# Optimization experiments

Measured on AMD Instinct MI355X. Metric: run time of the kernel, lower is better.

## Reference

```python
import jax, jax.numpy as jnp
import numpy as np

N = 4096          # num_nodes
F = 64            # node_features
H = 128           # hidden_dim
NH = 4            # num_heads
HD = H // NH      # per-head dim = 32
L = 3             # num_layers
C = 7             # num_classes
EDGE_P = 0.004    # ~16 avg degree


def setup_inputs() -> dict:
    key = jax.random.key(0)
    ks = jax.random.split(key, 20)
    g = lambda k, shape, fan_in: jax.random.normal(k, shape, jnp.float32) / np.sqrt(fan_in)
    x = jax.random.normal(ks[0], (N, F), jnp.float32)
    adj = (jax.random.uniform(ks[1], (N, N)) < EDGE_P).astype(jnp.float32)
    return {
        "x": x,
        "adj": adj,
        "enc_W": g(ks[2], (F, H), F), "enc_b": jnp.zeros((H,), jnp.float32),
        "gcn_W": g(ks[3], (L, H, H), H), "gcn_b": jnp.zeros((L, H), jnp.float32),
        "attn_W": g(ks[4], (L, NH, H, HD), H), "attn_Wb": jnp.zeros((L, NH, HD), jnp.float32),
        "attn_a": g(ks[5], (L, NH, 2 * HD), 2 * HD), "attn_ab": jnp.zeros((L, NH), jnp.float32),
        "cls_W1": g(ks[6], (H, H // 2), H), "cls_b1": jnp.zeros((H // 2,), jnp.float32),
        "cls_W2": g(ks[7], (H // 2, C), H // 2), "cls_b2": jnp.zeros((C,), jnp.float32),
        "con_W1": g(ks[8], (H, H // 2), H), "con_b1": jnp.zeros((H // 2,), jnp.float32),
        "con_W2": g(ks[9], (H // 2, 1), H // 2), "con_b2": jnp.zeros((1,), jnp.float32),
    }


def _normalize_adj(adj):
    a = adj + jnp.eye(adj.shape[0], dtype=adj.dtype)
    dinv = jnp.sum(a, axis=1) ** -0.5
    return dinv[:, None] * a * dinv[None, :]


def _gcn(h, adj_norm, W, b):
    support = adj_norm @ h                      # [N,H]
    return jax.nn.relu(support @ W + b)         # dropout=0 (eval)


def _attention(h, edge_mask, W, Wb, a, ab):
    # h:[N,H], W:[NH,H,HD], a:[NH,2*HD]; per-pair score = Linear(concat(h_i,h_j))
    hh = jnp.einsum('nf,hfd->hnd', h, W) + Wb[:, None, :]     # [NH,N,HD]
    a_src, a_dst = a[:, :HD], a[:, HD:]
    s_src = jnp.einsum('hnd,hd->hn', hh, a_src)               # [NH,N]
    s_dst = jnp.einsum('hnd,hd->hn', hh, a_dst)               # [NH,N]
    scores = s_src[:, :, None] + s_dst[:, None, :] + ab[:, None, None]
    # original uses literal 0.0 (NOT -inf) for non-edges before softmax
    scores = jnp.where(edge_mask[None, :, :], scores, 0.0)    # [NH,N,N]
    probs = jax.nn.softmax(scores, axis=-1)
    out = jnp.einsum('hij,hjd->hid', probs, hh)               # [NH,N,HD]
    return out.transpose(1, 0, 2).reshape(h.shape[0], NH * HD)


def reference(x, adj, enc_W, enc_b, gcn_W, gcn_b, attn_W, attn_Wb, attn_a, attn_ab,
              cls_W1, cls_b1, cls_W2, cls_b2, con_W1, con_b1, con_W2, con_b2):
    h = jax.nn.relu(x @ enc_W + enc_b)          # node encoder (dropout=0)
    adj_norm = _normalize_adj(adj)
    edge_mask = adj > 0
    for i in range(L):
        h_gcn = _gcn(h, adj_norm, gcn_W[i], gcn_b[i])
        h_attn = _attention(h, edge_mask, attn_W[i], attn_Wb[i], attn_a[i], attn_ab[i])
        h = jax.nn.relu(h_gcn + h_attn)
    node_logits = jax.nn.relu(h @ cls_W1 + cls_b1) @ cls_W2 + cls_b2
    h_mean = jnp.mean(h, axis=0, keepdims=True)
    contagion = jax.nn.relu(h_mean @ con_W1 + con_b1) @ con_W2 + con_b2
    return (node_logits, h, contagion)
```

## Files before the change

### kernel.cpp

```cpp
#include <hip/hip_runtime.h>

typedef unsigned short u16;
typedef unsigned int u32;

#define N 4096
#define F 64
#define H 128
#define NH 4
#define HD 32
#define EMAX 64

__device__ float g_hA[N * H];
__device__ float g_hB[N * H];
__device__ float g_hhA[N * H];
__device__ float g_hhB[N * H];
__device__ u16   g_cols[N * EMAX];
__device__ int   g_deg[N];
__device__ float g_dinv[N];
__device__ float g_ssrcA[N * NH];
__device__ float g_ssrcB[N * NH];
__device__ float g_sdstA[N * NH];
__device__ float g_sdstB[N * NH];
__device__ float g_part[4][32][H];
__device__ float g_gWQ[3 * H * H];
__device__ float g_aWQ[3 * NH * H * HD];
__device__ float g_W1Q[H * 64];

__device__ __forceinline__ void agg4(int i0, int tid, const float* __restrict__ h,
                                     const float* __restrict__ hhin,
                                     const float* __restrict__ ssrc_in,
                                     const float* __restrict__ sdst_in,
                                     int l, const float* __restrict__ abv,
                                     int (&jl)[4][EMAX], float (&dv)[4][EMAX],
                                     float (&sdl)[4][EMAX * NH], float (&wl)[4][EMAX * NH],
                                     float (&eml)[4][NH], float (&basel)[4][NH],
                                     float (&Svl)[4][NH],
                                     float& outa0, float& outa1,
                                     float& sup0, float& sup1) {
  int c = tid & 127, rg = tid >> 7, hc = c >> 5;
#pragma unroll
  for (int r = 0; r < 4; ++r) {
    int dd = g_deg[i0 + r];
    const u16* cl = g_cols + (size_t)(i0 + r) * EMAX;
    for (int e = tid; e < dd; e += 256) {
      int j = cl[e];
      jl[r][e] = j;
      dv[r][e] = g_dinv[j];
    }
  }
  __syncthreads();

  {
    int g = tid >> 4, lg = tid & 15, ra = g >> 2, ha = g & 3;
    int dda = g_deg[i0 + ra];
    float M = -INFINITY;
    for (int e = lg; e < dda; e += 16) {
      float s = sdst_in[jl[ra][e] * NH + ha];
      sdl[ra][e * NH + ha] = s;
      M = fmaxf(M, s);
    }
#pragma unroll
    for (int m = 8; m >= 1; m >>= 1) M = fmaxf(M, __shfl_xor(M, m, 64));
    if (lg == 0) {
      float ssrc = ssrc_in[(i0 + ra) * NH + ha];
      float ab = abv[ha];
      float mv = fmaxf(0.f, ssrc + ab + M);
      eml[ra][ha] = expf(-mv);
      basel[ra][ha] = ssrc + ab - mv;
    }
  }
  __syncthreads();

  {
    int g = tid >> 4, lg = tid & 15, ra = g >> 2, ha = g & 3;
    int dda = g_deg[i0 + ra];
    float base = basel[ra][ha];
    float Sp = 0.f;
    for (int e = lg; e < dda; e += 16) {
      float w = expf(base + sdl[ra][e * NH + ha]);
      wl[ra][e * NH + ha] = w;
      Sp += w;
    }
#pragma unroll
    for (int m = 8; m >= 1; m >>= 1) Sp += __shfl_xor(Sp, m, 64);
    if (lg == 0) Svl[ra][ha] = Sp;
  }
  __syncthreads();

  float sumc = 0.f;
  const float* part = &g_part[l][0][0];
#pragma unroll
  for (int s = 0; s < 32; ++s) sumc += part[s * H + c];

  float oa[2], sp[2];
#pragma unroll
  for (int rr = 0; rr < 2; ++rr) {
    int r = rg * 2 + rr;
    int i = i0 + r;
    int dd = g_deg[i];
    float em = eml[r][hc], S = Svl[r][hc];
    float aA = 0.f, aT = 0.f, aG = 0.f;
    int e = 0;
    for (; e + 4 <= dd; e += 4) {
      int j0 = jl[r][e], j1 = jl[r][e + 1], j2 = jl[r][e + 2], j3 = jl[r][e + 3];
      float w0 = wl[r][e * NH + hc],       w1 = wl[r][(e + 1) * NH + hc];
      float w2 = wl[r][(e + 2) * NH + hc], w3 = wl[r][(e + 3) * NH + hc];
      float q0 = hhin[j0 * H + c], q1 = hhin[j1 * H + c];
      float q2 = hhin[j2 * H + c], q3 = hhin[j3 * H + c];
      float p0 = h[j0 * H + c], p1 = h[j1 * H + c];
      float p2 = h[j2 * H + c], p3 = h[j3 * H + c];
      aA = fmaf(w0, q0, aA); aA = fmaf(w1, q1, aA);
      aA = fmaf(w2, q2, aA); aA = fmaf(w3, q3, aA);
      aT += (q0 + q1) + (q2 + q3);
      aG = fmaf(dv[r][e], p0, aG);     aG = fmaf(dv[r][e + 1], p1, aG);
      aG = fmaf(dv[r][e + 2], p2, aG); aG = fmaf(dv[r][e + 3], p3, aG);
    }
    for (; e < dd; ++e) {
      int j = jl[r][e];
      float w = wl[r][e * NH + hc];
      float q = hhin[j * H + c];
      aA = fmaf(w, q, aA);
      aT += q;
      aG = fmaf(dv[r][e], h[j * H + c], aG);
    }
    float Z = S + em * (float)(N - dd);
    oa[rr] = (aA + em * (sumc - aT)) / Z;
    float di = g_dinv[i];
    sp[rr] = di * (aG + di * h[i * H + c]);
  }
  outa0 = oa[0]; outa1 = oa[1]; sup0 = sp[0]; sup1 = sp[1];
}

__device__ __forceinline__ void proj4(int i0, int tid, const float (&hrowT)[H][4],
                                      const float* __restrict__ aW,
                                      const float* __restrict__ aWb,
                                      const float* __restrict__ aa, int lp,
                                      float* __restrict__ hhout,
                                      float* __restrict__ ssrc_out,
                                      float* __restrict__ sdst_out) {
  int c = tid & 127, rg = tid >> 7, hc = c >> 5, dc = c & 31;
  float b = aWb[hc * HD + dc];
  float p0 = b, p1 = b;
  for (int f = 0; f < H; ++f) {
    float w = aW[(hc * H + f) * HD + dc];
    float2 hv = *reinterpret_cast<const float2*>(&hrowT[f][rg * 2]);
    p0 = fmaf(hv.x, w, p0);
    p1 = fmaf(hv.y, w, p1);
  }
  int r0 = i0 + rg * 2, r1 = r0 + 1;
  hhout[r0 * H + c] = p0;
  hhout[r1 * H + c] = p1;
  const float* ap = aa + hc * 2 * HD;
  float as = ap[dc], ad = ap[HD + dc];
  float ss0 = p0 * as, ss1 = p1 * as, sd0 = p0 * ad, sd1 = p1 * ad;
#pragma unroll
  for (int m = 16; m >= 1; m >>= 1) {
    ss0 += __shfl_xor(ss0, m, 64); ss1 += __shfl_xor(ss1, m, 64);
    sd0 += __shfl_xor(sd0, m, 64); sd1 += __shfl_xor(sd1, m, 64);
  }
  if (dc == 0) {
    ssrc_out[r0 * NH + hc] = ss0; ssrc_out[r1 * NH + hc] = ss1;
    sdst_out[r0 * NH + hc] = sd0; sdst_out[r1 * NH + hc] = sd1;
  }
  atomicAdd(&g_part[lp][r0 & 31][c], p0);
  atomicAdd(&g_part[lp][r1 & 31][c], p1);
}

__global__ void k_csr_enc(const float* __restrict__ adj, const float* __restrict__ x,
                          const float* __restrict__ eW, const float* __restrict__ eb,
                          const float* __restrict__ aW, const float* __restrict__ aWb,
                          const float* __restrict__ aa, const float* __restrict__ gW,
                          const float* __restrict__ W1) {
  __shared__ float xT[F][4];
  __shared__ float hrowT[H][4];
  __shared__ int cnt;
  int tid = threadIdx.x;
  if (blockIdx.x < N) {
    int row = blockIdx.x;
    if (tid == 0) cnt = 0;
    __syncthreads();
    int base = tid * 16;
    const float4* p = reinterpret_cast<const float4*>(adj + (size_t)row * N + base);
    float4 q0 = p[0], q1 = p[1], q2 = p[2], q3 = p[3];
    float vals[16] = {q0.x, q0.y, q0.z, q0.w, q1.x, q1.y, q1.z, q1.w,
                      q2.x, q2.y, q2.z, q2.w, q3.x, q3.y, q3.z, q3.w};
#pragma unroll
    for (int t = 0; t < 16; ++t)
      if (vals[t] != 0.f) {
        int pos = atomicAdd(&cnt, 1);
        if (pos < EMAX) g_cols[row * EMAX + pos] = (u16)(base + t);
      }
    __syncthreads();
    if (tid == 0) {
      g_deg[row] = cnt < EMAX ? cnt : EMAX;
      g_dinv[row] = 1.0f / sqrtf((float)(cnt + 1));
    }
  } else if (blockIdx.x < N + N / 4) {
    int i0 = (blockIdx.x - N) * 4;
    int c = tid & 127, rg = tid >> 7;
    {
      int r = tid >> 6, k = tid & 63;
      xT[k][r] = x[(i0 + r) * F + k];
    }
    __syncthreads();
    float b = eb[c];
    float e0 = b, e1 = b;
    for (int k = 0; k < F; ++k) {
      float w = eW[k * H + c];
      float2 xv = *reinterpret_cast<const float2*>(&xT[k][rg * 2]);
      e0 = fmaf(xv.x, w, e0);
      e1 = fmaf(xv.y, w, e1);
    }
    e0 = fmaxf(e0, 0.f); e1 = fmaxf(e1, 0.f);
    int r0 = i0 + rg * 2, r1 = r0 + 1;
    g_hA[r0 * H + c] = e0; g_hA[r1 * H + c] = e1;
    hrowT[c][rg * 2] = e0; hrowT[c][rg * 2 + 1] = e1;
    __syncthreads();
    proj4(i0, tid, hrowT, aW, aWb, aa, 0, g_hhA, g_ssrcA, g_sdstA);
  } else {
    int gid = (blockIdx.x - (N + N / 4)) * 256 + tid;
    if (gid < 3 * H * H) {
      int l = gid / (H * H), rem = gid % (H * H);
      int fq = rem >> 9, c = (rem >> 2) & 127, ft = rem & 3;
      g_gWQ[gid] = gW[(size_t)l * H * H + (4 * fq + ft) * H + c];
      int hc = c >> 5, dc = c & 31;
      g_aWQ[gid] = aW[(((size_t)l * NH + hc) * H + (4 * fq + ft)) * HD + dc];
      if (gid < H * 64) {
        int fq2 = gid >> 8, u = (gid >> 2) & 63, ft2 = gid & 3;
        g_W1Q[gid] = W1[(4 * fq2 + ft2) * 64 + u];
      }
    }
  }
}

__device__ __forceinline__ void gemm2q(const float* __restrict__ s0,
                                       const float* __restrict__ s1,
                                       const float4* __restrict__ wq,
                                       float& a0, float& a1) {
#pragma unroll 4
  for (int fq = 0; fq < 32; ++fq) {
    float4 w  = wq[fq * 128];
    float4 v0 = *reinterpret_cast<const float4*>(s0 + fq * 4);
    float4 v1 = *reinterpret_cast<const float4*>(s1 + fq * 4);
    a0 = fmaf(v0.x, w.x, a0); a0 = fmaf(v0.y, w.y, a0);
    a0 = fmaf(v0.z, w.z, a0); a0 = fmaf(v0.w, w.w, a0);
    a1 = fmaf(v1.x, w.x, a1); a1 = fmaf(v1.y, w.y, a1);
    a1 = fmaf(v1.z, w.z, a1); a1 = fmaf(v1.w, w.w, a1);
  }
}

__device__ __forceinline__ void proj4q(int i0, int tid, const float (&hT)[4][H],
                                       const float4* __restrict__ aq,
                                       const float* __restrict__ aWb,
                                       const float* __restrict__ aa, int lp,
                                       float* __restrict__ hhout,
                                       float* __restrict__ ssrc_out,
                                       float* __restrict__ sdst_out) {
  int c = tid & 127, rg = tid >> 7, hc = c >> 5, dc = c & 31;
  float b = aWb[hc * HD + dc];
  float p0 = b, p1 = b;
  gemm2q(hT[rg * 2], hT[rg * 2 + 1], aq, p0, p1);
  int r0 = i0 + rg * 2, r1 = r0 + 1;
  hhout[r0 * H + c] = p0;
  hhout[r1 * H + c] = p1;
  const float* ap = aa + hc * 2 * HD;
  float as = ap[dc], ad = ap[HD + dc];
  float ss0 = p0 * as, ss1 = p1 * as, sd0 = p0 * ad, sd1 = p1 * ad;
#pragma unroll
  for (int m = 16; m >= 1; m >>= 1) {
    ss0 += __shfl_xor(ss0, m, 64); ss1 += __shfl_xor(ss1, m, 64);
    sd0 += __shfl_xor(sd0, m, 64); sd1 += __shfl_xor(sd1, m, 64);
  }
  if (dc == 0) {
    ssrc_out[r0 * NH + hc] = ss0; ssrc_out[r1 * NH + hc] = ss1;
    sdst_out[r0 * NH + hc] = sd0; sdst_out[r1 * NH + hc] = sd1;
  }
  atomicAdd(&g_part[lp][r0 & 31][c], p0);
  atomicAdd(&g_part[lp][r1 & 31][c], p1);
}

__global__ void k_acp(int pp, int l, const float* __restrict__ gb,
                      const float* __restrict__ aWb, const float* __restrict__ aa,
                      const float* __restrict__ abv) {
  const float* h    = pp ? g_hB : g_hA;
  float*       hout = pp ? g_hA : g_hB;
  const float* hhin = pp ? g_hhB : g_hhA;
  float*       hhout= pp ? g_hhA : g_hhB;
  const float* ssin = pp ? g_ssrcB : g_ssrcA;
  float*       ssout= pp ? g_ssrcA : g_ssrcB;
  const float* sdin = pp ? g_sdstB : g_sdstA;
  float*       sdout= pp ? g_sdstA : g_sdstB;
  __shared__ int   jl[4][EMAX];
  __shared__ float dv[4][EMAX];
  __shared__ float sdl[4][EMAX * NH];
  __shared__ float wl[4][EMAX * NH];
  __shared__ float eml[4][NH], basel[4][NH], Svl[4][NH];
  __shared__ float sT[4][H];
  __shared__ float hT[4][H];
  int i0 = blockIdx.x * 4, tid = threadIdx.x;
  int c = tid & 127, rg = tid >> 7;

  float oa0, oa1, sp0, sp1;
  agg4(i0, tid, h, hhin, ssin, sdin, l, abv, jl, dv, sdl, wl, eml, basel, Svl,
       oa0, oa1, sp0, sp1);
  sT[rg * 2][c] = sp0; sT[rg * 2 + 1][c] = sp1;
  __syncthreads();

  float b = gb[c];
  float a0 = b, a1 = b;
  const float4* gq = reinterpret_cast<const float4*>(g_gWQ) + (size_t)l * 4096 + c;
  gemm2q(sT[rg * 2], sT[rg * 2 + 1], gq, a0, a1);
  float g0 = fmaxf(fmaxf(a0, 0.f) + oa0, 0.f);
  float g1 = fmaxf(fmaxf(a1, 0.f) + oa1, 0.f);
  int r0 = i0 + rg * 2, r1 = r0 + 1;
  hout[r0 * H + c] = g0; hout[r1 * H + c] = g1;
  hT[rg * 2][c] = g0; hT[rg * 2 + 1][c] = g1;
  __syncthreads();

  const float4* aq = reinterpret_cast<const float4*>(g_aWQ) + (size_t)(l + 1) * 4096 + c;
  proj4q(i0, tid, hT, aq, aWb, aa, l + 1, hhout, ssout, sdout);
}

__global__ void k_acc(const float* __restrict__ abv, const float* __restrict__ gb,
                      const float* __restrict__ b1,
                      const float* __restrict__ W2, const float* __restrict__ b2,
                      float* __restrict__ out, float* __restrict__ outh) {
  __shared__ int   jl[4][EMAX];
  __shared__ float dv[4][EMAX];
  __shared__ float sdl[4][EMAX * NH];
  __shared__ float wl[4][EMAX * NH];
  __shared__ float eml[4][NH], basel[4][NH], Svl[4][NH];
  __shared__ float sT[4][H];
  __shared__ float hT[4][H];
  __shared__ float tl[4][64];
  int i0 = blockIdx.x * 4, tid = threadIdx.x;
  int c = tid & 127, rg = tid >> 7;

  float oa0, oa1, sp0, sp1;
  agg4(i0, tid, g_hA, g_hhA, g_ssrcA, g_sdstA, 2, abv, jl, dv, sdl, wl, eml, basel,
       Svl, oa0, oa1, sp0, sp1);
  sT[rg * 2][c] = sp0; sT[rg * 2 + 1][c] = sp1;
  __syncthreads();

  float b = gb[c];
  float a0 = b, a1 = b;
  const float4* gq = reinterpret_cast<const float4*>(g_gWQ) + (size_t)2 * 4096 + c;
  gemm2q(sT[rg * 2], sT[rg * 2 + 1], gq, a0, a1);
  float g0 = fmaxf(fmaxf(a0, 0.f) + oa0, 0.f);
  float g1 = fmaxf(fmaxf(a1, 0.f) + oa1, 0.f);
  int r0 = i0 + rg * 2, r1 = r0 + 1;
  outh[r0 * H + c] = g0; outh[r1 * H + c] = g1;
  hT[rg * 2][c] = g0; hT[rg * 2 + 1][c] = g1;
  atomicAdd(&g_part[3][r0 & 31][c], g0);
  atomicAdd(&g_part[3][r1 & 31][c], g1);
  __syncthreads();

  int u = tid & 63, rr4 = tid >> 6;
  float a2 = b1[u];
  {
    const float4* w1q = reinterpret_cast<const float4*>(g_W1Q) + u;
    const float* hr = hT[rr4];
#pragma unroll 4
    for (int fq = 0; fq < 32; ++fq) {
      float4 w  = w1q[fq * 64];
      float4 hv = *reinterpret_cast<const float4*>(hr + fq * 4);
      a2 = fmaf(hv.x, w.x, a2); a2 = fmaf(hv.y, w.y, a2);
      a2 = fmaf(hv.z, w.z, a2); a2 = fmaf(hv.w, w.w, a2);
    }
  }
  tl[rr4][u] = fmaxf(a2, 0.f);
  __syncthreads();
  if (tid < 28) {
    int r = tid / 7, j = tid - r * 7;
    float p = b2[j];
    for (int v = 0; v < 64; ++v) p = fmaf(tl[r][v], W2[v * 7 + j], p);
    out[(i0 + r) * 7 + j] = p;
  }
}

__global__ void k_contagion(const float* __restrict__ W1, const float* __restrict__ b1,
                            const float* __restrict__ W2, const float* __restrict__ b2,
                            float* __restrict__ out) {
  __shared__ float hm[H];
  __shared__ float tl[64];
  int u = threadIdx.x;
#pragma unroll
  for (int q = 0; q < 2; ++q) {
    int col = u + q * 64;
    float s = 0.f;
#pragma unroll
    for (int sl = 0; sl < 32; ++sl) s += g_part[3][sl][col];
    hm[col] = s * (1.0f / 4096.0f);
  }
  __syncthreads();
  float acc = b1[u];
  for (int f = 0; f < H; ++f) acc = fmaf(hm[f], W1[f * 64 + u], acc);
  tl[u] = fmaxf(acc, 0.f);
  __syncthreads();
  if (u == 0) {
    float p = b2[0];
    for (int v = 0; v < 64; ++v) p = fmaf(tl[v], W2[v], p);
    out[0] = p;
  }
}

extern "C" void kernel_launch(void* const* d_in, const int* in_sizes, int n_in,
                              void* d_out, int out_size, void* d_ws, size_t ws_size,
                              hipStream_t stream) {
  const float* x       = (const float*)d_in[0];
  const float* adj     = (const float*)d_in[1];
  const float* enc_W   = (const float*)d_in[2];
  const float* enc_b   = (const float*)d_in[3];
  const float* gcn_W   = (const float*)d_in[4];
  const float* gcn_b   = (const float*)d_in[5];
  const float* attn_W  = (const float*)d_in[6];
  const float* attn_Wb = (const float*)d_in[7];
  const float* attn_a  = (const float*)d_in[8];
  const float* attn_ab = (const float*)d_in[9];
  const float* cls_W1  = (const float*)d_in[10];
  const float* cls_b1  = (const float*)d_in[11];
  const float* cls_W2  = (const float*)d_in[12];
  const float* cls_b2  = (const float*)d_in[13];
  const float* con_W1  = (const float*)d_in[14];
  const float* con_b1  = (const float*)d_in[15];
  const float* con_W2  = (const float*)d_in[16];
  const float* con_b2  = (const float*)d_in[17];
  (void)in_sizes; (void)n_in; (void)d_ws; (void)ws_size; (void)out_size;

  float* out = (float*)d_out;
  float* outh = out + (size_t)N * 7;
  float* outc = out + (size_t)N * 7 + (size_t)N * H;

  void* zr = nullptr;
  hipGetSymbolAddress(&zr, HIP_SYMBOL(g_part));
  hipMemsetAsync(zr, 0, sizeof(float) * 4 * 32 * H, stream);

  k_csr_enc<<<N + N / 4 + 192, 256, 0, stream>>>(adj, x, enc_W, enc_b,
                                                 attn_W, attn_Wb, attn_a,
                                                 gcn_W, cls_W1);
  k_acp<<<N / 4, 256, 0, stream>>>(0, 0, gcn_b,
                                   attn_Wb + (size_t)1 * NH * HD,
                                   attn_a + (size_t)1 * NH * 2 * HD, attn_ab);
  k_acp<<<N / 4, 256, 0, stream>>>(1, 1, gcn_b + H,
                                   attn_Wb + (size_t)2 * NH * HD,
                                   attn_a + (size_t)2 * NH * 2 * HD, attn_ab + NH);
  k_acc<<<N / 4, 256, 0, stream>>>(attn_ab + 2 * NH, gcn_b + 2 * H,
                                   cls_b1, cls_W2, cls_b2, out, outh);
  k_contagion<<<1, 64, 0, stream>>>(con_W1, con_b1, con_W2, con_b2, outc);
}
```

Before: 218.9 us.

## Pack node features with projections and give each aggregation row one wavefront

```diff
diff --git a/kernel.cpp b/kernel.cpp
--- a/kernel.cpp
+++ b/kernel.cpp
@@ -1,7 +1,6 @@
 #include <hip/hip_runtime.h>
 
 typedef unsigned short u16;
-typedef unsigned int u32;
 
 #define N 4096
 #define F 64
@@ -10,10 +9,8 @@
 #define HD 32
 #define EMAX 64
 
-__device__ float g_hA[N * H];
-__device__ float g_hB[N * H];
-__device__ float g_hhA[N * H];
-__device__ float g_hhB[N * H];
+__device__ float2 g_pkA[N * H];
+__device__ float2 g_pkB[N * H];
 __device__ u16   g_cols[N * EMAX];
 __device__ int   g_deg[N];
 __device__ float g_dinv[N];
@@ -26,118 +23,116 @@
 __device__ float g_aWQ[3 * NH * H * HD];
 __device__ float g_W1Q[H * 64];
 
-__device__ __forceinline__ void agg4(int i0, int tid, const float* __restrict__ h,
-                                     const float* __restrict__ hhin,
-                                     const float* __restrict__ ssrc_in,
-                                     const float* __restrict__ sdst_in,
+__device__ __forceinline__ void agg4(int i0, int tid, const float2* __restrict__ pk,
+                                     const float* __restrict__ ssin,
+                                     const float* __restrict__ sdin,
                                      int l, const float* __restrict__ abv,
                                      int (&jl)[4][EMAX], float (&dv)[4][EMAX],
-                                     float (&sdl)[4][EMAX * NH], float (&wl)[4][EMAX * NH],
-                                     float (&eml)[4][NH], float (&basel)[4][NH],
-                                     float (&Svl)[4][NH],
-                                     float& outa0, float& outa1,
-                                     float& sup0, float& sup1) {
-  int c = tid & 127, rg = tid >> 7, hc = c >> 5;
-#pragma unroll
-  for (int r = 0; r < 4; ++r) {
-    int dd = g_deg[i0 + r];
-    const u16* cl = g_cols + (size_t)(i0 + r) * EMAX;
-    for (int e = tid; e < dd; e += 256) {
-      int j = cl[e];
-      jl[r][e] = j;
-      dv[r][e] = g_dinv[j];
-    }
-  }
-  __syncthreads();
-
-  {
-    int g = tid >> 4, lg = tid & 15, ra = g >> 2, ha = g & 3;
-    int dda = g_deg[i0 + ra];
-    float M = -INFINITY;
-    for (int e = lg; e < dda; e += 16) {
-      float s = sdst_in[jl[ra][e] * NH + ha];
-      sdl[ra][e * NH + ha] = s;
-      M = fmaxf(M, s);
-    }
-#pragma unroll
-    for (int m = 8; m >= 1; m >>= 1) M = fmaxf(M, __shfl_xor(M, m, 64));
-    if (lg == 0) {
-      float ssrc = ssrc_in[(i0 + ra) * NH + ha];
-      float ab = abv[ha];
-      float mv = fmaxf(0.f, ssrc + ab + M);
-      eml[ra][ha] = expf(-mv);
-      basel[ra][ha] = ssrc + ab - mv;
-    }
-  }
-  __syncthreads();
-
-  {
-    int g = tid >> 4, lg = tid & 15, ra = g >> 2, ha = g & 3;
-    int dda = g_deg[i0 + ra];
-    float base = basel[ra][ha];
-    float Sp = 0.f;
-    for (int e = lg; e < dda; e += 16) {
-      float w = expf(base + sdl[ra][e * NH + ha]);
-      wl[ra][e * NH + ha] = w;
+                                     float (&wl)[4][EMAX * NH],
+                                     float (&oaT)[4][H], float (&spT)[4][H]) {
+  int r = tid >> 6;
+  int t = tid & 63;
+  int hc = t >> 4;
+  int lg = t & 15;
+  int i = i0 + r;
+  int dd = g_deg[i];
+
+  if (t < dd) {
+    int j = g_cols[(size_t)i * EMAX + t];
+    jl[r][t] = j;
+    dv[r][t] = g_dinv[j];
+  }
+
+  float sreg[4];
+  float M = -INFINITY;
+#pragma unroll
+  for (int k = 0; k < 4; ++k) {
+    int e = lg + 16 * k;
+    float s = -INFINITY;
+    if (e < dd) s = sdin[jl[r][e] * NH + hc];
+    sreg[k] = s;
+    M = fmaxf(M, s);
+  }
+#pragma unroll
+  for (int m = 8; m >= 1; m >>= 1) M = fmaxf(M, __shfl_xor(M, m, 64));
+
+  float ssrc = ssin[i * NH + hc];
+  float ab = abv[hc];
+  float mv = fmaxf(0.f, ssrc + ab + M);
+  float em = expf(-mv);
+  float base = ssrc + ab - mv;
+
+  float Sp = 0.f;
+#pragma unroll
+  for (int k = 0; k < 4; ++k) {
+    int e = lg + 16 * k;
+    if (e < dd) {
+      float w = expf(base + sreg[k]);
+      wl[r][e * NH + hc] = w;
       Sp += w;
     }
-#pragma unroll
-    for (int m = 8; m >= 1; m >>= 1) Sp += __shfl_xor(Sp, m, 64);
-    if (lg == 0) Svl[ra][ha] = Sp;
-  }
-  __syncthreads();
-
-  float sumc = 0.f;
-  const float* part = &g_part[l][0][0];
-#pragma unroll
-  for (int s = 0; s < 32; ++s) sumc += part[s * H + c];
-
-  float oa[2], sp[2];
-#pragma unroll
-  for (int rr = 0; rr < 2; ++rr) {
-    int r = rg * 2 + rr;
-    int i = i0 + r;
-    int dd = g_deg[i];
-    float em = eml[r][hc], S = Svl[r][hc];
-    float aA = 0.f, aT = 0.f, aG = 0.f;
-    int e = 0;
-    for (; e + 4 <= dd; e += 4) {
-      int j0 = jl[r][e], j1 = jl[r][e + 1], j2 = jl[r][e + 2], j3 = jl[r][e + 3];
-      float w0 = wl[r][e * NH + hc],       w1 = wl[r][(e + 1) * NH + hc];
-      float w2 = wl[r][(e + 2) * NH + hc], w3 = wl[r][(e + 3) * NH + hc];
-      float q0 = hhin[j0 * H + c], q1 = hhin[j1 * H + c];
-      float q2 = hhin[j2 * H + c], q3 = hhin[j3 * H + c];
-      float p0 = h[j0 * H + c], p1 = h[j1 * H + c];
-      float p2 = h[j2 * H + c], p3 = h[j3 * H + c];
-      aA = fmaf(w0, q0, aA); aA = fmaf(w1, q1, aA);
-      aA = fmaf(w2, q2, aA); aA = fmaf(w3, q3, aA);
-      aT += (q0 + q1) + (q2 + q3);
-      aG = fmaf(dv[r][e], p0, aG);     aG = fmaf(dv[r][e + 1], p1, aG);
-      aG = fmaf(dv[r][e + 2], p2, aG); aG = fmaf(dv[r][e + 3], p3, aG);
-    }
-    for (; e < dd; ++e) {
-      int j = jl[r][e];
-      float w = wl[r][e * NH + hc];
-      float q = hhin[j * H + c];
-      aA = fmaf(w, q, aA);
-      aT += q;
-      aG = fmaf(dv[r][e], h[j * H + c], aG);
-    }
-    float Z = S + em * (float)(N - dd);
-    oa[rr] = (aA + em * (sumc - aT)) / Z;
-    float di = g_dinv[i];
-    sp[rr] = di * (aG + di * h[i * H + c]);
-  }
-  outa0 = oa[0]; outa1 = oa[1]; sup0 = sp[0]; sup1 = sp[1];
-}
-
-__device__ __forceinline__ void proj4(int i0, int tid, const float (&hrowT)[H][4],
-                                      const float* __restrict__ aW,
-                                      const float* __restrict__ aWb,
-                                      const float* __restrict__ aa, int lp,
-                                      float* __restrict__ hhout,
-                                      float* __restrict__ ssrc_out,
-                                      float* __restrict__ sdst_out) {
+  }
+#pragma unroll
+  for (int m = 8; m >= 1; m >>= 1) Sp += __shfl_xor(Sp, m, 64);
+  float S = Sp;
+
+  const float2* ps = reinterpret_cast<const float2*>(&g_part[l][0][0]) + t;
+  float sc0 = 0.f, sc1 = 0.f;
+#pragma unroll
+  for (int s = 0; s < 32; ++s) {
+    float2 v = ps[s * 64];
+    sc0 += v.x;
+    sc1 += v.y;
+  }
+
+  float aA0 = 0.f, aA1 = 0.f, aT0 = 0.f, aT1 = 0.f, aG0 = 0.f, aG1 = 0.f;
+  int e = 0;
+  for (; e + 4 <= dd; e += 4) {
+    int j0 = jl[r][e], j1 = jl[r][e + 1], j2 = jl[r][e + 2], j3 = jl[r][e + 3];
+    float4 v0 = *reinterpret_cast<const float4*>(pk + (size_t)j0 * H + 2 * t);
+    float4 v1 = *reinterpret_cast<const float4*>(pk + (size_t)j1 * H + 2 * t);
+    float4 v2 = *reinterpret_cast<const float4*>(pk + (size_t)j2 * H + 2 * t);
+    float4 v3 = *reinterpret_cast<const float4*>(pk + (size_t)j3 * H + 2 * t);
+    float w0 = wl[r][e * NH + hc],       w1 = wl[r][(e + 1) * NH + hc];
+    float w2 = wl[r][(e + 2) * NH + hc], w3 = wl[r][(e + 3) * NH + hc];
+    float d0 = dv[r][e], d1 = dv[r][e + 1], d2 = dv[r][e + 2], d3 = dv[r][e + 3];
+    aA0 = fmaf(w0, v0.y, aA0); aA0 = fmaf(w1, v1.y, aA0);
+    aA0 = fmaf(w2, v2.y, aA0); aA0 = fmaf(w3, v3.y, aA0);
+    aA1 = fmaf(w0, v0.w, aA1); aA1 = fmaf(w1, v1.w, aA1);
+    aA1 = fmaf(w2, v2.w, aA1); aA1 = fmaf(w3, v3.w, aA1);
+    aT0 += (v0.y + v1.y) + (v2.y + v3.y);
+    aT1 += (v0.w + v1.w) + (v2.w + v3.w);
+    aG0 = fmaf(d0, v0.x, aG0); aG0 = fmaf(d1, v1.x, aG0);
+    aG0 = fmaf(d2, v2.x, aG0); aG0 = fmaf(d3, v3.x, aG0);
+    aG1 = fmaf(d0, v0.z, aG1); aG1 = fmaf(d1, v1.z, aG1);
+    aG1 = fmaf(d2, v2.z, aG1); aG1 = fmaf(d3, v3.z, aG1);
+  }
+  for (; e < dd; ++e) {
+    int j = jl[r][e];
+    float4 v = *reinterpret_cast<const float4*>(pk + (size_t)j * H + 2 * t);
+    float w = wl[r][e * NH + hc];
+    float d = dv[r][e];
+    aA0 = fmaf(w, v.y, aA0); aA1 = fmaf(w, v.w, aA1);
+    aT0 += v.y;              aT1 += v.w;
+    aG0 = fmaf(d, v.x, aG0); aG1 = fmaf(d, v.z, aG1);
+  }
+  float Z = S + em * (float)(N - dd);
+  float4 vs = *reinterpret_cast<const float4*>(pk + (size_t)i * H + 2 * t);
+  float di = g_dinv[i];
+  oaT[r][2 * t]     = (aA0 + em * (sc0 - aT0)) / Z;
+  oaT[r][2 * t + 1] = (aA1 + em * (sc1 - aT1)) / Z;
+  spT[r][2 * t]     = di * (aG0 + di * vs.x);
+  spT[r][2 * t + 1] = di * (aG1 + di * vs.z);
+}
+
+__device__ __forceinline__ void proj4pk(int i0, int tid, const float (&hrowT)[H][4],
+                                        const float* __restrict__ aW,
+                                        const float* __restrict__ aWb,
+                                        const float* __restrict__ aa, int lp,
+                                        float hv0, float hv1,
+                                        float2* __restrict__ pkout,
+                                        float* __restrict__ ssrc_out,
+                                        float* __restrict__ sdst_out) {
   int c = tid & 127, rg = tid >> 7, hc = c >> 5, dc = c & 31;
   float b = aWb[hc * HD + dc];
   float p0 = b, p1 = b;
@@ -148,8 +143,55 @@
     p1 = fmaf(hv.y, w, p1);
   }
   int r0 = i0 + rg * 2, r1 = r0 + 1;
-  hhout[r0 * H + c] = p0;
-  hhout[r1 * H + c] = p1;
+  pkout[(size_t)r0 * H + c] = make_float2(hv0, p0);
+  pkout[(size_t)r1 * H + c] = make_float2(hv1, p1);
+  const float* ap = aa + hc * 2 * HD;
+  float as = ap[dc], ad = ap[HD + dc];
+  float ss0 = p0 * as, ss1 = p1 * as, sd0 = p0 * ad, sd1 = p1 * ad;
+#pragma unroll
+  for (int m = 16; m >= 1; m >>= 1) {
+    ss0 += __shfl_xor(ss0, m, 64); ss1 += __shfl_xor(ss1, m, 64);
+    sd0 += __shfl_xor(sd0, m, 64); sd1 += __shfl_xor(sd1, m, 64);
+  }
+  if (dc == 0) {
+    ssrc_out[r0 * NH + hc] = ss0; ssrc_out[r1 * NH + hc] = ss1;
+    sdst_out[r0 * NH + hc] = sd0; sdst_out[r1 * NH + hc] = sd1;
+  }
+  atomicAdd(&g_part[lp][r0 & 31][c], p0);
+  atomicAdd(&g_part[lp][r1 & 31][c], p1);
+}
+
+__device__ __forceinline__ void gemm2q(const float* __restrict__ s0,
+                                       const float* __restrict__ s1,
+                                       const float4* __restrict__ wq,
+                                       float& a0, float& a1) {
+#pragma unroll 4
+  for (int fq = 0; fq < 32; ++fq) {
+    float4 w  = wq[fq * 128];
+    float4 v0 = *reinterpret_cast<const float4*>(s0 + fq * 4);
+    float4 v1 = *reinterpret_cast<const float4*>(s1 + fq * 4);
+    a0 = fmaf(v0.x, w.x, a0); a0 = fmaf(v0.y, w.y, a0);
+    a0 = fmaf(v0.z, w.z, a0); a0 = fmaf(v0.w, w.w, a0);
+    a1 = fmaf(v1.x, w.x, a1); a1 = fmaf(v1.y, w.y, a1);
+    a1 = fmaf(v1.z, w.z, a1); a1 = fmaf(v1.w, w.w, a1);
+  }
+}
+
+__device__ __forceinline__ void proj4qpk(int i0, int tid, const float (&hT)[4][H],
+                                         const float4* __restrict__ aq,
+                                         const float* __restrict__ aWb,
+                                         const float* __restrict__ aa, int lp,
+                                         float g0v, float g1v,
+                                         float2* __restrict__ pkout,
+                                         float* __restrict__ ssrc_out,
+                                         float* __restrict__ sdst_out) {
+  int c = tid & 127, rg = tid >> 7, hc = c >> 5, dc = c & 31;
+  float b = aWb[hc * HD + dc];
+  float p0 = b, p1 = b;
+  gemm2q(hT[rg * 2], hT[rg * 2 + 1], aq, p0, p1);
+  int r0 = i0 + rg * 2, r1 = r0 + 1;
+  pkout[(size_t)r0 * H + c] = make_float2(g0v, p0);
+  pkout[(size_t)r1 * H + c] = make_float2(g1v, p1);
   const float* ap = aa + hc * 2 * HD;
   float as = ap[dc], ad = ap[HD + dc];
   float ss0 = p0 * as, ss1 = p1 * as, sd0 = p0 * ad, sd1 = p1 * ad;
@@ -200,7 +242,7 @@
     int c = tid & 127, rg = tid >> 7;
     {
       int r = tid >> 6, k = tid & 63;
-      xT[k][r] = x[(i0 + r) * F + k];
+      xT[k][r] = x[(size_t)(i0 + r) * F + k];
     }
     __syncthreads();
     float b = eb[c];
@@ -212,19 +254,17 @@
       e1 = fmaf(xv.y, w, e1);
     }
     e0 = fmaxf(e0, 0.f); e1 = fmaxf(e1, 0.f);
-    int r0 = i0 + rg * 2, r1 = r0 + 1;
-    g_hA[r0 * H + c] = e0; g_hA[r1 * H + c] = e1;
     hrowT[c][rg * 2] = e0; hrowT[c][rg * 2 + 1] = e1;
     __syncthreads();
-    proj4(i0, tid, hrowT, aW, aWb, aa, 0, g_hhA, g_ssrcA, g_sdstA);
+    proj4pk(i0, tid, hrowT, aW, aWb, aa, 0, e0, e1, g_pkA, g_ssrcA, g_sdstA);
   } else {
     int gid = (blockIdx.x - (N + N / 4)) * 256 + tid;
     if (gid < 3 * H * H) {
       int l = gid / (H * H), rem = gid % (H * H);
-      int fq = rem >> 9, c = (rem >> 2) & 127, ft = rem & 3;
-      g_gWQ[gid] = gW[(size_t)l * H * H + (4 * fq + ft) * H + c];
-      int hc = c >> 5, dc = c & 31;
-      g_aWQ[gid] = aW[(((size_t)l * NH + hc) * H + (4 * fq + ft)) * HD + dc];
+      int fq = rem >> 9, cc = (rem >> 2) & 127, ft = rem & 3;
+      g_gWQ[gid] = gW[(size_t)l * H * H + (4 * fq + ft) * H + cc];
+      int hc2 = cc >> 5, dc2 = cc & 31;
+      g_aWQ[gid] = aW[(((size_t)l * NH + hc2) * H + (4 * fq + ft)) * HD + dc2];
       if (gid < H * 64) {
         int fq2 = gid >> 8, u = (gid >> 2) & 63, ft2 = gid & 3;
         g_W1Q[gid] = W1[(4 * fq2 + ft2) * 64 + u];
@@ -233,92 +273,38 @@
   }
 }
 
-__device__ __forceinline__ void gemm2q(const float* __restrict__ s0,
-                                       const float* __restrict__ s1,
-                                       const float4* __restrict__ wq,
-                                       float& a0, float& a1) {
-#pragma unroll 4
-  for (int fq = 0; fq < 32; ++fq) {
-    float4 w  = wq[fq * 128];
-    float4 v0 = *reinterpret_cast<const float4*>(s0 + fq * 4);
-    float4 v1 = *reinterpret_cast<const float4*>(s1 + fq * 4);
-    a0 = fmaf(v0.x, w.x, a0); a0 = fmaf(v0.y, w.y, a0);
-    a0 = fmaf(v0.z, w.z, a0); a0 = fmaf(v0.w, w.w, a0);
-    a1 = fmaf(v1.x, w.x, a1); a1 = fmaf(v1.y, w.y, a1);
-    a1 = fmaf(v1.z, w.z, a1); a1 = fmaf(v1.w, w.w, a1);
-  }
-}
-
-__device__ __forceinline__ void proj4q(int i0, int tid, const float (&hT)[4][H],
-                                       const float4* __restrict__ aq,
-                                       const float* __restrict__ aWb,
-                                       const float* __restrict__ aa, int lp,
-                                       float* __restrict__ hhout,
-                                       float* __restrict__ ssrc_out,
-                                       float* __restrict__ sdst_out) {
-  int c = tid & 127, rg = tid >> 7, hc = c >> 5, dc = c & 31;
-  float b = aWb[hc * HD + dc];
-  float p0 = b, p1 = b;
-  gemm2q(hT[rg * 2], hT[rg * 2 + 1], aq, p0, p1);
-  int r0 = i0 + rg * 2, r1 = r0 + 1;
-  hhout[r0 * H + c] = p0;
-  hhout[r1 * H + c] = p1;
-  const float* ap = aa + hc * 2 * HD;
-  float as = ap[dc], ad = ap[HD + dc];
-  float ss0 = p0 * as, ss1 = p1 * as, sd0 = p0 * ad, sd1 = p1 * ad;
-#pragma unroll
-  for (int m = 16; m >= 1; m >>= 1) {
-    ss0 += __shfl_xor(ss0, m, 64); ss1 += __shfl_xor(ss1, m, 64);
-    sd0 += __shfl_xor(sd0, m, 64); sd1 += __shfl_xor(sd1, m, 64);
-  }
-  if (dc == 0) {
-    ssrc_out[r0 * NH + hc] = ss0; ssrc_out[r1 * NH + hc] = ss1;
-    sdst_out[r0 * NH + hc] = sd0; sdst_out[r1 * NH + hc] = sd1;
-  }
-  atomicAdd(&g_part[lp][r0 & 31][c], p0);
-  atomicAdd(&g_part[lp][r1 & 31][c], p1);
-}
-
 __global__ void k_acp(int pp, int l, const float* __restrict__ gb,
                       const float* __restrict__ aWb, const float* __restrict__ aa,
                       const float* __restrict__ abv) {
-  const float* h    = pp ? g_hB : g_hA;
-  float*       hout = pp ? g_hA : g_hB;
-  const float* hhin = pp ? g_hhB : g_hhA;
-  float*       hhout= pp ? g_hhA : g_hhB;
-  const float* ssin = pp ? g_ssrcB : g_ssrcA;
-  float*       ssout= pp ? g_ssrcA : g_ssrcB;
-  const float* sdin = pp ? g_sdstB : g_sdstA;
-  float*       sdout= pp ? g_sdstA : g_sdstB;
+  const float2* pk    = pp ? g_pkB : g_pkA;
+  float2*       pkout = pp ? g_pkA : g_pkB;
+  const float*  ssin  = pp ? g_ssrcB : g_ssrcA;
+  float*        ssout = pp ? g_ssrcA : g_ssrcB;
+  const float*  sdin  = pp ? g_sdstB : g_sdstA;
+  float*        sdout = pp ? g_sdstA : g_sdstB;
   __shared__ int   jl[4][EMAX];
   __shared__ float dv[4][EMAX];
-  __shared__ float sdl[4][EMAX * NH];
   __shared__ float wl[4][EMAX * NH];
-  __shared__ float eml[4][NH], basel[4][NH], Svl[4][NH];
-  __shared__ float sT[4][H];
+  __shared__ float oaT[4][H];
+  __shared__ float spT[4][H];
   __shared__ float hT[4][H];
   int i0 = blockIdx.x * 4, tid = threadIdx.x;
   int c = tid & 127, rg = tid >> 7;
 
-  float oa0, oa1, sp0, sp1;
-  agg4(i0, tid, h, hhin, ssin, sdin, l, abv, jl, dv, sdl, wl, eml, basel, Svl,
-       oa0, oa1, sp0, sp1);
-  sT[rg * 2][c] = sp0; sT[rg * 2 + 1][c] = sp1;
-  __syncthreads();
-
-  float b = gb[c];
-  float a0 = b, a1 = b;
+  agg4(i0, tid, pk, ssin, sdin, l, abv, jl, dv, wl, oaT, spT);
+  __syncthreads();
+
+  float bb = gb[c];
+  float a0 = bb, a1 = bb;
   const float4* gq = reinterpret_cast<const float4*>(g_gWQ) + (size_t)l * 4096 + c;
-  gemm2q(sT[rg * 2], sT[rg * 2 + 1], gq, a0, a1);
-  float g0 = fmaxf(fmaxf(a0, 0.f) + oa0, 0.f);
-  float g1 = fmaxf(fmaxf(a1, 0.f) + oa1, 0.f);
-  int r0 = i0 + rg * 2, r1 = r0 + 1;
-  hout[r0 * H + c] = g0; hout[r1 * H + c] = g1;
+  gemm2q(spT[rg * 2], spT[rg * 2 + 1], gq, a0, a1);
+  float g0 = fmaxf(fmaxf(a0, 0.f) + oaT[rg * 2][c], 0.f);
+  float g1 = fmaxf(fmaxf(a1, 0.f) + oaT[rg * 2 + 1][c], 0.f);
   hT[rg * 2][c] = g0; hT[rg * 2 + 1][c] = g1;
   __syncthreads();
 
   const float4* aq = reinterpret_cast<const float4*>(g_aWQ) + (size_t)(l + 1) * 4096 + c;
-  proj4q(i0, tid, hT, aq, aWb, aa, l + 1, hhout, ssout, sdout);
+  proj4qpk(i0, tid, hT, aq, aWb, aa, l + 1, g0, g1, pkout, ssout, sdout);
 }
 
 __global__ void k_acc(const float* __restrict__ abv, const float* __restrict__ gb,
@@ -327,29 +313,26 @@
                       float* __restrict__ out, float* __restrict__ outh) {
   __shared__ int   jl[4][EMAX];
   __shared__ float dv[4][EMAX];
-  __shared__ float sdl[4][EMAX * NH];
   __shared__ float wl[4][EMAX * NH];
-  __shared__ float eml[4][NH], basel[4][NH], Svl[4][NH];
-  __shared__ float sT[4][H];
+  __shared__ float oaT[4][H];
+  __shared__ float spT[4][H];
   __shared__ float hT[4][H];
   __shared__ float tl[4][64];
   int i0 = blockIdx.x * 4, tid = threadIdx.x;
   int c = tid & 127, rg = tid >> 7;
 
-  float oa0, oa1, sp0, sp1;
-  agg4(i0, tid, g_hA, g_hhA, g_ssrcA, g_sdstA, 2, abv, jl, dv, sdl, wl, eml, basel,
-       Svl, oa0, oa1, sp0, sp1);
-  sT[rg * 2][c] = sp0; sT[rg * 2 + 1][c] = sp1;
-  __syncthreads();
-
-  float b = gb[c];
-  float a0 = b, a1 = b;
+  agg4(i0, tid, g_pkA, g_ssrcA, g_sdstA, 2, abv, jl, dv, wl, oaT, spT);
+  __syncthreads();
+
+  float bb = gb[c];
+  float a0 = bb, a1 = bb;
   const float4* gq = reinterpret_cast<const float4*>(g_gWQ) + (size_t)2 * 4096 + c;
-  gemm2q(sT[rg * 2], sT[rg * 2 + 1], gq, a0, a1);
-  float g0 = fmaxf(fmaxf(a0, 0.f) + oa0, 0.f);
-  float g1 = fmaxf(fmaxf(a1, 0.f) + oa1, 0.f);
+  gemm2q(spT[rg * 2], spT[rg * 2 + 1], gq, a0, a1);
+  float g0 = fmaxf(fmaxf(a0, 0.f) + oaT[rg * 2][c], 0.f);
+  float g1 = fmaxf(fmaxf(a1, 0.f) + oaT[rg * 2 + 1][c], 0.f);
   int r0 = i0 + rg * 2, r1 = r0 + 1;
-  outh[r0 * H + c] = g0; outh[r1 * H + c] = g1;
+  outh[(size_t)r0 * H + c] = g0;
+  outh[(size_t)r1 * H + c] = g1;
   hT[rg * 2][c] = g0; hT[rg * 2 + 1][c] = g1;
   atomicAdd(&g_part[3][r0 & 31][c], g0);
   atomicAdd(&g_part[3][r1 & 31][c], g1);
@@ -374,7 +357,7 @@
     int r = tid / 7, j = tid - r * 7;
     float p = b2[j];
     for (int v = 0; v < 64; ++v) p = fmaf(tl[r][v], W2[v * 7 + j], p);
-    out[(i0 + r) * 7 + j] = p;
+    out[(size_t)(i0 + r) * 7 + j] = p;
   }
 }
 
```

Result: faster. 214.1 us (-2.2%).
